# Kernel tuning notes

Hardware: AMD Instinct MI355X
Metric: run time of the kernel (lower is better)

Reference implementation:

```python
import jax, jax.numpy as jnp
import numpy as np

D_MODEL = 1024
N_HEADS = 16
HEAD_DIM = D_MODEL // N_HEADS
B, L = 2, 2048


def setup_inputs() -> dict:
    key = jax.random.key(0)
    ks = jax.random.split(key, 12)
    s = 1.0 / np.sqrt(D_MODEL)
    inp = {
        'q': jax.random.normal(ks[0], (B, L, D_MODEL), dtype=jnp.float32),
        'k': jax.random.normal(ks[1], (B, L, D_MODEL), dtype=jnp.float32),
        'v': jax.random.normal(ks[2], (B, L, D_MODEL), dtype=jnp.float32),
        'Wq': jax.random.uniform(ks[3], (D_MODEL, D_MODEL), jnp.float32, -s, s),
        'bq': jax.random.uniform(ks[4], (D_MODEL,), jnp.float32, -s, s),
        'Wk': jax.random.uniform(ks[5], (D_MODEL, D_MODEL), jnp.float32, -s, s),
        'bk': jax.random.uniform(ks[6], (D_MODEL,), jnp.float32, -s, s),
        'Wv': jax.random.uniform(ks[7], (D_MODEL, D_MODEL), jnp.float32, -s, s),
        'bv': jax.random.uniform(ks[8], (D_MODEL,), jnp.float32, -s, s),
        'Wo': jax.random.uniform(ks[9], (D_MODEL, D_MODEL), jnp.float32, -s, s),
        'bo': jax.random.uniform(ks[10], (D_MODEL,), jnp.float32, -s, s),
    }
    return inp


def _heads(x):
    # (B, L, D) -> (B, H, L, Dh)
    b, l, _ = x.shape
    return x.reshape(b, l, N_HEADS, HEAD_DIM).transpose(0, 2, 1, 3)


def reference(q, k, v, Wq, bq, Wk, bk, Wv, bv, Wo, bo):
    # Linear projections (torch Linear: x @ W.T + b)
    qh = _heads(q @ Wq.T + bq)
    kh = _heads(k @ Wk.T + bk)
    vh = _heads(v @ Wv.T + bv)
    scale = 1.0 / jnp.sqrt(jnp.asarray(HEAD_DIM, dtype=qh.dtype))
    scores = jnp.einsum('bhqd,bhkd->bhqk', qh, kh) * scale  # (B,H,L,L)
    attn = jax.nn.softmax(scores, axis=-1)
    out = jnp.einsum('bhqk,bhkd->bhqd', attn, vh)
    out = out.transpose(0, 2, 1, 3).reshape(q.shape[0], q.shape[1], D_MODEL)
    return out @ Wo.T + bo
```

## Files before the change

### kernel.cpp

```cpp
#include <hip/hip_runtime.h>

typedef unsigned short u16;
typedef __bf16 bf16x8 __attribute__((ext_vector_type(8)));
typedef float f32x4 __attribute__((ext_vector_type(4)));
typedef float f32x16 __attribute__((ext_vector_type(16)));
typedef unsigned short u16x8 __attribute__((ext_vector_type(8)));
typedef unsigned short u16x4 __attribute__((ext_vector_type(4)));

#define LSEQ 2048
#define DM 1024
#define NH 16
#define HD 64
#define SCALE_Q 0.1803368801111244f

__device__ __forceinline__ u16 f2bf(float f) {
  union { float f; unsigned int u; } x;
  x.f = f;
  unsigned int u = x.u;
  u += 0x7FFFu + ((u >> 16) & 1u);
  return (u16)(u >> 16);
}

__device__ __forceinline__ float fexp2(float x) {
  return __builtin_amdgcn_exp2f(x);
}

__device__ __forceinline__ void async16(const void* g, void* l) {
  __builtin_amdgcn_global_load_lds(
      (const __attribute__((address_space(1))) void*)g,
      (__attribute__((address_space(3))) void*)l, 16, 0, 0);
}

__device__ __forceinline__ f32x4 mfma16(bf16x8 a, bf16x8 b, f32x4 c) {
  return __builtin_amdgcn_mfma_f32_16x16x32_bf16(a, b, c, 0, 0, 0);
}
__device__ __forceinline__ f32x16 mfma32(bf16x8 a, bf16x8 b, f32x16 c) {
  return __builtin_amdgcn_mfma_f32_32x32x16_bf16(a, b, c, 0, 0, 0);
}

__device__ __forceinline__ unsigned cvtpk(float lo, float hi) {
  unsigned r;
  asm("v_cvt_pk_bf16_f32 %0, %1, %2" : "=v"(r) : "v"(lo), "v"(hi));
  return r;
}
__device__ __forceinline__ void pswap(unsigned &a, unsigned &b) {
  asm("v_permlane32_swap_b32 %0, %1" : "+v"(a), "+v"(b));
}
__device__ __forceinline__ bf16x8 mk8(unsigned w0, unsigned w1, unsigned w2, unsigned w3) {
  union { unsigned u[4]; bf16x8 v; } x;
  x.u[0] = w0; x.u[1] = w1; x.u[2] = w2; x.u[3] = w3;
  return x.v;
}
__device__ __forceinline__ f32x16 zero16() {
  f32x16 z;
#pragma unroll
  for (int i = 0; i < 16; ++i) z[i] = 0.f;
  return z;
}

__global__ void cvtw(const float* __restrict__ src, u16* __restrict__ dst, int n) {
  const int i = (blockIdx.x * blockDim.x + threadIdx.x) * 4;
  if (i >= n) return;
  f32x4 f = *(const f32x4*)(src + i);
  u16x4 h;
#pragma unroll
  for (int j = 0; j < 4; ++j) h[j] = f2bf(f[j]);
  *(u16x4*)(dst + i) = h;
}

__global__ __launch_bounds__(256) void gemm_qkv(
    const float* __restrict__ xq, const float* __restrict__ xk, const float* __restrict__ xv,
    const u16* __restrict__ Wqb, const u16* __restrict__ Wkb, const u16* __restrict__ Wvb,
    const float* __restrict__ bq, const float* __restrict__ bk, const float* __restrict__ bv,
    u16* __restrict__ Qp, u16* __restrict__ Kp, u16* __restrict__ Vp)
{
  __shared__ __align__(16) u16 As[2][128 * 32];
  __shared__ __align__(16) u16 Bs[2][128 * 32];

  const int tid = threadIdx.x;
  const int lane = tid & 63;
  const int wid = tid >> 6;
  const int lr = lane & 15, lg = lane >> 4;
  const int wr = wid >> 1, wc = wid & 1;
  const int bm = blockIdx.x;
  const int by = blockIdx.y;
  const int wsel = by >> 3;
  const int bn = by & 7;

  const float* A    = (wsel == 0) ? xq  : (wsel == 1) ? xk  : xv;
  const u16*   Bt   = (wsel == 0) ? Wqb : (wsel == 1) ? Wkb : Wvb;
  const float* bias = (wsel == 0) ? bq  : (wsel == 1) ? bk  : bv;
  u16*         Out  = (wsel == 0) ? Qp  : (wsel == 1) ? Kp  : Vp;
  const float oscale = (wsel == 0) ? SCALE_Q : 1.0f;

  const int r0 = tid >> 2;
  const int c0 = (tid & 3) * 8;
  const size_t arow0 = (size_t)(bm * 128 + r0) * DM;
  const size_t arow1 = (size_t)(bm * 128 + 64 + r0) * DM;
  const size_t brow0 = (size_t)(bn * 128 + r0) * DM;
  const size_t brow1 = (size_t)(bn * 128 + 64 + r0) * DM;

  f32x4 acc[4][4];
#pragma unroll
  for (int m = 0; m < 4; ++m)
#pragma unroll
    for (int n = 0; n < 4; ++n) {
      f32x4 z = {0.f, 0.f, 0.f, 0.f};
      acc[m][n] = z;
    }

  {
    async16(Bt + brow0 + c0, &Bs[0][tid * 8]);
    async16(Bt + brow1 + c0, &Bs[0][2048 + tid * 8]);
    const float* g0 = A + arow0 + c0;
    const float* g1 = A + arow1 + c0;
    f32x4 v00 = *(const f32x4*)g0, v01 = *(const f32x4*)(g0 + 4);
    f32x4 v10 = *(const f32x4*)g1, v11 = *(const f32x4*)(g1 + 4);
    u16x8 h0, h1;
#pragma unroll
    for (int j = 0; j < 4; ++j) {
      h0[j] = f2bf(v00[j]); h0[4 + j] = f2bf(v01[j]);
      h1[j] = f2bf(v10[j]); h1[4 + j] = f2bf(v11[j]);
    }
    *(u16x8*)&As[0][tid * 8] = h0;
    *(u16x8*)&As[0][2048 + tid * 8] = h1;
  }
  __syncthreads();

  for (int kt = 0; kt < 32; ++kt) {
    const int cur = kt & 1, nxt = cur ^ 1;
    const bool hn = (kt + 1) < 32;
    f32x4 v00, v01, v10, v11;
    if (hn) {
      const int kk = (kt + 1) * 32;
      async16(Bt + brow0 + kk + c0, &Bs[nxt][tid * 8]);
      async16(Bt + brow1 + kk + c0, &Bs[nxt][2048 + tid * 8]);
      const float* g0 = A + arow0 + kk + c0;
      const float* g1 = A + arow1 + kk + c0;
      v00 = *(const f32x4*)g0; v01 = *(const f32x4*)(g0 + 4);
      v10 = *(const f32x4*)g1; v11 = *(const f32x4*)(g1 + 4);
    }
    bf16x8 af[4], bfr[4];
#pragma unroll
    for (int m = 0; m < 4; ++m)
      af[m] = *(const bf16x8*)&As[cur][(wr * 64 + m * 16 + lr) * 32 + lg * 8];
#pragma unroll
    for (int n = 0; n < 4; ++n)
      bfr[n] = *(const bf16x8*)&Bs[cur][(wc * 64 + n * 16 + lr) * 32 + lg * 8];
#pragma unroll
    for (int m = 0; m < 4; ++m)
#pragma unroll
      for (int n = 0; n < 4; ++n)
        acc[m][n] = mfma16(af[m], bfr[n], acc[m][n]);
    if (hn) {
      u16x8 h0, h1;
#pragma unroll
      for (int j = 0; j < 4; ++j) {
        h0[j] = f2bf(v00[j]); h0[4 + j] = f2bf(v01[j]);
        h1[j] = f2bf(v10[j]); h1[4 + j] = f2bf(v11[j]);
      }
      *(u16x8*)&As[nxt][tid * 8] = h0;
      *(u16x8*)&As[nxt][2048 + tid * 8] = h1;
    }
    __syncthreads();
  }

#pragma unroll
  for (int m = 0; m < 4; ++m) {
#pragma unroll
    for (int n = 0; n < 4; ++n) {
      const int col = bn * 128 + wc * 64 + n * 16 + lr;
      const float bv_ = bias[col];
      const int h = col >> 6, d = col & 63;
#pragma unroll
      for (int r = 0; r < 4; ++r) {
        const int row = bm * 128 + wr * 64 + m * 16 + lg * 4 + r;
        const int b = row >> 11, l = row & 2047;
        Out[((size_t)(b * NH + h) * LSEQ + l) * HD + d] =
            f2bf((acc[m][n][r] + bv_) * oscale);
      }
    }
  }
}

__global__ __launch_bounds__(256) void attn_fwd(
    const u16* __restrict__ Qp, const u16* __restrict__ Kp, const u16* __restrict__ Vp,
    u16* __restrict__ ctx)
{
  __shared__ __align__(16) u16 Ks[2][64 * 64];
  __shared__ __align__(16) u16 Vts[2][64 * 64];

  const int tid = threadIdx.x;
  const int wid = tid >> 6;
  const int lane = tid & 63;
  const int lq = lane & 31;
  const int h = lane >> 5;
  const int qt = blockIdx.x, bh = blockIdx.y;

  const u16* Qb = Qp + (size_t)bh * (LSEQ * HD);
  const u16* Kb = Kp + (size_t)bh * (LSEQ * HD);
  const u16* Vb = Vp + (size_t)bh * (LSEQ * HD);

  const int q0 = qt * 128 + wid * 32;

  bf16x8 qf[4];
#pragma unroll
  for (int dk = 0; dk < 4; ++dk)
    qf[dk] = *(const bf16x8*)(Qb + (size_t)(q0 + lq) * HD + dk * 16 + h * 8);

  float l_run = 0.f;
  f32x16 o0 = zero16(), o1 = zero16();

  const int krow = tid >> 3;
  const int kslot = tid & 7;
  const int ksrc = krow * 64 + ((kslot ^ (krow & 7)) << 3);

  const int kp = tid & 31;
  const int vd0 = (tid >> 5) * 8;

  {
    async16(Kb + ksrc, &Ks[0][tid * 8]);
    async16(Kb + 2048 + ksrc, &Ks[0][2048 + tid * 8]);
    const u16* vsrc = Vb + (size_t)(2 * kp) * HD + vd0;
    u16x8 va = *(const u16x8*)vsrc;
    u16x8 vb_ = *(const u16x8*)(vsrc + HD);
    unsigned int* V32 = (unsigned int*)&Vts[0][0];
#pragma unroll
    for (int i = 0; i < 8; ++i) {
      const int row = vd0 + i;
      V32[row * 32 + (kp ^ ((row & 7) << 2))] =
          (unsigned int)va[i] | ((unsigned int)vb_[i] << 16);
    }
  }
  __syncthreads();

  for (int kt = 0; kt < LSEQ / 64; ++kt) {
    const int cur = kt & 1, nxt = cur ^ 1;
    const bool hn = (kt + 1) < LSEQ / 64;
    u16x8 va, vb_;
    if (hn) {
      async16(Kb + (kt + 1) * 4096 + ksrc, &Ks[nxt][tid * 8]);
      async16(Kb + (kt + 1) * 4096 + 2048 + ksrc, &Ks[nxt][2048 + tid * 8]);
      const u16* vsrc = Vb + (size_t)((kt + 1) * 64 + 2 * kp) * HD + vd0;
      va = *(const u16x8*)vsrc;
      vb_ = *(const u16x8*)(vsrc + HD);
    }

    f32x16 st0 = zero16(), st1 = zero16();
    __builtin_amdgcn_s_setprio(1);
#pragma unroll
    for (int dk = 0; dk < 4; ++dk) {
      const int g = ((2 * dk + h) ^ (lq & 7)) << 3;
      bf16x8 kf0 = *(const bf16x8*)&Ks[cur][lq * 64 + g];
      bf16x8 kf1 = *(const bf16x8*)&Ks[cur][(32 + lq) * 64 + g];
      st0 = mfma32(kf0, qf[dk], st0);
      st1 = mfma32(kf1, qf[dk], st1);
    }
    __builtin_amdgcn_s_setprio(0);

    float rs = 0.f;
#pragma unroll
    for (int i = 0; i < 16; ++i) { st0[i] = fexp2(st0[i]); rs += st0[i]; }
#pragma unroll
    for (int i = 0; i < 16; ++i) { st1[i] = fexp2(st1[i]); rs += st1[i]; }
    l_run += rs;

    unsigned w[16];
#pragma unroll
    for (int m = 0; m < 4; ++m) {
      w[m * 2 + 0] = cvtpk(st0[4 * m + 0], st0[4 * m + 1]);
      w[m * 2 + 1] = cvtpk(st0[4 * m + 2], st0[4 * m + 3]);
      w[8 + m * 2 + 0] = cvtpk(st1[4 * m + 0], st1[4 * m + 1]);
      w[8 + m * 2 + 1] = cvtpk(st1[4 * m + 2], st1[4 * m + 3]);
    }
#pragma unroll
    for (int n = 0; n < 2; ++n) {
      pswap(w[n * 8 + 0], w[n * 8 + 2]);
      pswap(w[n * 8 + 1], w[n * 8 + 3]);
      pswap(w[n * 8 + 4], w[n * 8 + 6]);
      pswap(w[n * 8 + 5], w[n * 8 + 7]);
    }
    bf16x8 pa[4];
    pa[0] = mk8(w[0], w[1], w[2], w[3]);
    pa[1] = mk8(w[4], w[5], w[6], w[7]);
    pa[2] = mk8(w[8], w[9], w[10], w[11]);
    pa[3] = mk8(w[12], w[13], w[14], w[15]);

    __builtin_amdgcn_s_setprio(1);
#pragma unroll
    for (int ks = 0; ks < 4; ++ks) {
      const int g0g = ((2 * ks + h) ^ (lq & 7)) << 3;
      bf16x8 vf0 = *(const bf16x8*)&Vts[cur][lq * 64 + g0g];
      bf16x8 vf1 = *(const bf16x8*)&Vts[cur][(32 + lq) * 64 + g0g];
      o0 = mfma32(pa[ks], vf0, o0);
      o1 = mfma32(pa[ks], vf1, o1);
    }
    __builtin_amdgcn_s_setprio(0);

    if (hn) {
      unsigned int* V32 = (unsigned int*)&Vts[nxt][0];
#pragma unroll
      for (int i = 0; i < 8; ++i) {
        const int row = vd0 + i;
        V32[row * 32 + (kp ^ ((row & 7) << 2))] =
            (unsigned int)va[i] | ((unsigned int)vb_[i] << 16);
      }
    }
    __syncthreads();
  }

  const int b = bh >> 4, head = bh & 15;
  const float ltot = l_run + __shfl_xor(l_run, 32);
  const float linv = 1.0f / ltot;
#pragma unroll
  for (int reg = 0; reg < 16; ++reg) {
    const int row = (reg & 3) + 8 * (reg >> 2) + 4 * h;
    const float iv = __shfl(linv, row);
    const size_t base = ((size_t)(b * LSEQ + q0 + row)) * DM + head * HD;
    ctx[base + lq] = f2bf(o0[reg] * iv);
    ctx[base + 32 + lq] = f2bf(o1[reg] * iv);
  }
}

__global__ __launch_bounds__(256) void gemm_out(
    const u16* __restrict__ Actx, const u16* __restrict__ Wob,
    const float* __restrict__ bo, float* __restrict__ out)
{
  __shared__ __align__(16) u16 As[2][128 * 32];
  __shared__ __align__(16) u16 Bs[2][128 * 32];

  const int tid = threadIdx.x;
  const int lane = tid & 63;
  const int wid = tid >> 6;
  const int lr = lane & 15, lg = lane >> 4;
  const int wr = wid >> 1, wc = wid & 1;
  const int bm = blockIdx.x;
  const int bn = blockIdx.y;

  const int r0 = tid >> 2;
  const int c0 = (tid & 3) * 8;
  const size_t arow0 = (size_t)(bm * 128 + r0) * DM;
  const size_t arow1 = (size_t)(bm * 128 + 64 + r0) * DM;
  const size_t brow0 = (size_t)(bn * 128 + r0) * DM;
  const size_t brow1 = (size_t)(bn * 128 + 64 + r0) * DM;

  f32x4 acc[4][4];
#pragma unroll
  for (int m = 0; m < 4; ++m)
#pragma unroll
    for (int n = 0; n < 4; ++n) {
      f32x4 z = {0.f, 0.f, 0.f, 0.f};
      acc[m][n] = z;
    }

  async16(Actx + arow0 + c0, &As[0][tid * 8]);
  async16(Actx + arow1 + c0, &As[0][2048 + tid * 8]);
  async16(Wob + brow0 + c0, &Bs[0][tid * 8]);
  async16(Wob + brow1 + c0, &Bs[0][2048 + tid * 8]);
  __syncthreads();

  for (int kt = 0; kt < 32; ++kt) {
    const int cur = kt & 1, nxt = cur ^ 1;
    if (kt + 1 < 32) {
      const int kk = (kt + 1) * 32;
      async16(Actx + arow0 + kk + c0, &As[nxt][tid * 8]);
      async16(Actx + arow1 + kk + c0, &As[nxt][2048 + tid * 8]);
      async16(Wob + brow0 + kk + c0, &Bs[nxt][tid * 8]);
      async16(Wob + brow1 + kk + c0, &Bs[nxt][2048 + tid * 8]);
    }
    bf16x8 af[4], bfr[4];
#pragma unroll
    for (int m = 0; m < 4; ++m)
      af[m] = *(const bf16x8*)&As[cur][(wr * 64 + m * 16 + lr) * 32 + lg * 8];
#pragma unroll
    for (int n = 0; n < 4; ++n)
      bfr[n] = *(const bf16x8*)&Bs[cur][(wc * 64 + n * 16 + lr) * 32 + lg * 8];
#pragma unroll
    for (int m = 0; m < 4; ++m)
#pragma unroll
      for (int n = 0; n < 4; ++n)
        acc[m][n] = mfma16(af[m], bfr[n], acc[m][n]);
    __syncthreads();
  }

#pragma unroll
  for (int m = 0; m < 4; ++m) {
#pragma unroll
    for (int n = 0; n < 4; ++n) {
      const int col = bn * 128 + wc * 64 + n * 16 + lr;
      const float bv_ = bo[col];
#pragma unroll
      for (int r = 0; r < 4; ++r) {
        const int row = bm * 128 + wr * 64 + m * 16 + lg * 4 + r;
        out[(size_t)row * DM + col] = acc[m][n][r] + bv_;
      }
    }
  }
}

extern "C" void kernel_launch(void* const* d_in, const int* in_sizes, int n_in,
                              void* d_out, int out_size, void* d_ws, size_t ws_size,
                              hipStream_t stream) {
  const float* q  = (const float*)d_in[0];
  const float* k  = (const float*)d_in[1];
  const float* v  = (const float*)d_in[2];
  const float* Wq = (const float*)d_in[3];
  const float* bq = (const float*)d_in[4];
  const float* Wk = (const float*)d_in[5];
  const float* bk = (const float*)d_in[6];
  const float* Wv = (const float*)d_in[7];
  const float* bv = (const float*)d_in[8];
  const float* Wo = (const float*)d_in[9];
  const float* bo = (const float*)d_in[10];
  float* out = (float*)d_out;

  u16* ws  = (u16*)d_ws;
  u16* Wqb = ws;
  u16* Wkb = Wqb + (1u << 20);
  u16* Wvb = Wkb + (1u << 20);
  u16* Wob = Wvb + (1u << 20);
  u16* Qp  = Wob + (1u << 20);
  u16* Kp  = Qp + (4u << 20);
  u16* Vp  = Kp + (4u << 20);
  u16* ctx = Vp + (4u << 20);

  cvtw<<<1024, 256, 0, stream>>>(Wq, Wqb, 1 << 20);
  cvtw<<<1024, 256, 0, stream>>>(Wk, Wkb, 1 << 20);
  cvtw<<<1024, 256, 0, stream>>>(Wv, Wvb, 1 << 20);
  cvtw<<<1024, 256, 0, stream>>>(Wo, Wob, 1 << 20);
  gemm_qkv<<<dim3(32, 24), 256, 0, stream>>>(q, k, v, Wqb, Wkb, Wvb,
                                             bq, bk, bv, Qp, Kp, Vp);
  attn_fwd<<<dim3(16, 32), 256, 0, stream>>>(Qp, Kp, Vp, ctx);
  gemm_out<<<dim3(32, 8), 256, 0, stream>>>(ctx, Wob, bo, out);
}
```

Before: 145.5 us.

## Write V transposed from projection GEMM and load it with async copies

The QKV projection now writes V directly in a transposed per-head layout (d-major, sequence contiguous) with packed bf16 stores. The attention kernel then fetches V tiles with the same swizzled async global-to-LDS copies used for K, instead of loading rows into registers and scattering transposed 32-bit writes into LDS every iteration. Separately, fp32-to-bf16 conversion in cvtw and in the GEMM A staging uses the packed hardware convert instruction and handles 8 elements per thread. The cost is strided 8-byte global stores for V in the GEMM epilogue. The packed convert may also round differently from the software round-to-nearest-even helper.

```diff
diff --git a/kernel.cpp b/kernel.cpp
--- a/kernel.cpp
+++ b/kernel.cpp
@@ -6,6 +6,8 @@
 typedef float f32x16 __attribute__((ext_vector_type(16)));
 typedef unsigned short u16x8 __attribute__((ext_vector_type(8)));
 typedef unsigned short u16x4 __attribute__((ext_vector_type(4)));
+typedef unsigned int u32x2 __attribute__((ext_vector_type(2)));
+typedef unsigned int u32x4 __attribute__((ext_vector_type(4)));
 
 #define LSEQ 2048
 #define DM 1024
@@ -57,22 +59,26 @@
   for (int i = 0; i < 16; ++i) z[i] = 0.f;
   return z;
 }
+__device__ __forceinline__ void pack8(const f32x4& a, const f32x4& b, void* dst) {
+  u32x4 w;
+  w[0] = cvtpk(a[0], a[1]); w[1] = cvtpk(a[2], a[3]);
+  w[2] = cvtpk(b[0], b[1]); w[3] = cvtpk(b[2], b[3]);
+  *(u32x4*)dst = w;
+}
 
 __global__ void cvtw(const float* __restrict__ src, u16* __restrict__ dst, int n) {
-  const int i = (blockIdx.x * blockDim.x + threadIdx.x) * 4;
+  const int i = (blockIdx.x * blockDim.x + threadIdx.x) * 8;
   if (i >= n) return;
-  f32x4 f = *(const f32x4*)(src + i);
-  u16x4 h;
-#pragma unroll
-  for (int j = 0; j < 4; ++j) h[j] = f2bf(f[j]);
-  *(u16x4*)(dst + i) = h;
+  f32x4 f0 = *(const f32x4*)(src + i);
+  f32x4 f1 = *(const f32x4*)(src + i + 4);
+  pack8(f0, f1, dst + i);
 }
 
 __global__ __launch_bounds__(256) void gemm_qkv(
     const float* __restrict__ xq, const float* __restrict__ xk, const float* __restrict__ xv,
     const u16* __restrict__ Wqb, const u16* __restrict__ Wkb, const u16* __restrict__ Wvb,
     const float* __restrict__ bq, const float* __restrict__ bk, const float* __restrict__ bv,
-    u16* __restrict__ Qp, u16* __restrict__ Kp, u16* __restrict__ Vp)
+    u16* __restrict__ Qp, u16* __restrict__ Kp, u16* __restrict__ Vt)
 {
   __shared__ __align__(16) u16 As[2][128 * 32];
   __shared__ __align__(16) u16 Bs[2][128 * 32];
@@ -90,8 +96,6 @@
   const float* A    = (wsel == 0) ? xq  : (wsel == 1) ? xk  : xv;
   const u16*   Bt   = (wsel == 0) ? Wqb : (wsel == 1) ? Wkb : Wvb;
   const float* bias = (wsel == 0) ? bq  : (wsel == 1) ? bk  : bv;
-  u16*         Out  = (wsel == 0) ? Qp  : (wsel == 1) ? Kp  : Vp;
-  const float oscale = (wsel == 0) ? SCALE_Q : 1.0f;
 
   const int r0 = tid >> 2;
   const int c0 = (tid & 3) * 8;
@@ -116,14 +120,8 @@
     const float* g1 = A + arow1 + c0;
     f32x4 v00 = *(const f32x4*)g0, v01 = *(const f32x4*)(g0 + 4);
     f32x4 v10 = *(const f32x4*)g1, v11 = *(const f32x4*)(g1 + 4);
-    u16x8 h0, h1;
-#pragma unroll
-    for (int j = 0; j < 4; ++j) {
-      h0[j] = f2bf(v00[j]); h0[4 + j] = f2bf(v01[j]);
-      h1[j] = f2bf(v10[j]); h1[4 + j] = f2bf(v11[j]);
-    }
-    *(u16x8*)&As[0][tid * 8] = h0;
-    *(u16x8*)&As[0][2048 + tid * 8] = h1;
+    pack8(v00, v01, &As[0][tid * 8]);
+    pack8(v10, v11, &As[0][2048 + tid * 8]);
   }
   __syncthreads();
 
@@ -153,38 +151,53 @@
       for (int n = 0; n < 4; ++n)
         acc[m][n] = mfma16(af[m], bfr[n], acc[m][n]);
     if (hn) {
-      u16x8 h0, h1;
-#pragma unroll
-      for (int j = 0; j < 4; ++j) {
-        h0[j] = f2bf(v00[j]); h0[4 + j] = f2bf(v01[j]);
-        h1[j] = f2bf(v10[j]); h1[4 + j] = f2bf(v11[j]);
+      pack8(v00, v01, &As[nxt][tid * 8]);
+      pack8(v10, v11, &As[nxt][2048 + tid * 8]);
+    }
+    __syncthreads();
+  }
+
+  if (wsel < 2) {
+    u16* Out = (wsel == 0) ? Qp : Kp;
+    const float oscale = (wsel == 0) ? SCALE_Q : 1.0f;
+#pragma unroll
+    for (int m = 0; m < 4; ++m) {
+#pragma unroll
+      for (int n = 0; n < 4; ++n) {
+        const int col = bn * 128 + wc * 64 + n * 16 + lr;
+        const float bv_ = bias[col];
+        const int h = col >> 6, d = col & 63;
+#pragma unroll
+        for (int r = 0; r < 4; ++r) {
+          const int row = bm * 128 + wr * 64 + m * 16 + lg * 4 + r;
+          const int b = row >> 11, l = row & 2047;
+          Out[((size_t)(b * NH + h) * LSEQ + l) * HD + d] =
+              f2bf((acc[m][n][r] + bv_) * oscale);
+        }
       }
-      *(u16x8*)&As[nxt][tid * 8] = h0;
-      *(u16x8*)&As[nxt][2048 + tid * 8] = h1;
-    }
-    __syncthreads();
-  }
-
-#pragma unroll
-  for (int m = 0; m < 4; ++m) {
-#pragma unroll
-    for (int n = 0; n < 4; ++n) {
-      const int col = bn * 128 + wc * 64 + n * 16 + lr;
-      const float bv_ = bias[col];
-      const int h = col >> 6, d = col & 63;
-#pragma unroll
-      for (int r = 0; r < 4; ++r) {
-        const int row = bm * 128 + wr * 64 + m * 16 + lg * 4 + r;
-        const int b = row >> 11, l = row & 2047;
-        Out[((size_t)(b * NH + h) * LSEQ + l) * HD + d] =
-            f2bf((acc[m][n][r] + bv_) * oscale);
+    }
+  } else {
+    const int row0b = bm * 128 + wr * 64 + lg * 4;
+    const int b = (bm * 128) >> 11;
+#pragma unroll
+    for (int m = 0; m < 4; ++m) {
+      const int l0 = (row0b + m * 16) & 2047;
+#pragma unroll
+      for (int n = 0; n < 4; ++n) {
+        const int col = bn * 128 + wc * 64 + n * 16 + lr;
+        const float bv_ = bias[col];
+        const int h = col >> 6, d = col & 63;
+        u32x2 w;
+        w[0] = cvtpk(acc[m][n][0] + bv_, acc[m][n][1] + bv_);
+        w[1] = cvtpk(acc[m][n][2] + bv_, acc[m][n][3] + bv_);
+        *(u32x2*)&Vt[((size_t)(b * NH + h) * HD + d) * LSEQ + l0] = w;
       }
     }
   }
 }
 
 __global__ __launch_bounds__(256) void attn_fwd(
-    const u16* __restrict__ Qp, const u16* __restrict__ Kp, const u16* __restrict__ Vp,
+    const u16* __restrict__ Qp, const u16* __restrict__ Kp, const u16* __restrict__ Vt,
     u16* __restrict__ ctx)
 {
   __shared__ __align__(16) u16 Ks[2][64 * 64];
@@ -199,7 +212,7 @@
 
   const u16* Qb = Qp + (size_t)bh * (LSEQ * HD);
   const u16* Kb = Kp + (size_t)bh * (LSEQ * HD);
-  const u16* Vb = Vp + (size_t)bh * (LSEQ * HD);
+  const u16* Vb = Vt + (size_t)bh * (HD * LSEQ);
 
   const int q0 = qt * 128 + wid * 32;
 
@@ -211,39 +224,29 @@
   float l_run = 0.f;
   f32x16 o0 = zero16(), o1 = zero16();
 
-  const int krow = tid >> 3;
-  const int kslot = tid & 7;
-  const int ksrc = krow * 64 + ((kslot ^ (krow & 7)) << 3);
-
-  const int kp = tid & 31;
-  const int vd0 = (tid >> 5) * 8;
+  const int srow = tid >> 3;
+  const int sslot = tid & 7;
+  const int sswz = (sslot ^ (srow & 7)) << 3;
+  const int ksrc = srow * 64 + sswz;
+  const size_t vsrc0 = (size_t)srow * LSEQ + sswz;
+  const size_t vsrc1 = (size_t)(srow + 32) * LSEQ + sswz;
 
   {
     async16(Kb + ksrc, &Ks[0][tid * 8]);
     async16(Kb + 2048 + ksrc, &Ks[0][2048 + tid * 8]);
-    const u16* vsrc = Vb + (size_t)(2 * kp) * HD + vd0;
-    u16x8 va = *(const u16x8*)vsrc;
-    u16x8 vb_ = *(const u16x8*)(vsrc + HD);
-    unsigned int* V32 = (unsigned int*)&Vts[0][0];
-#pragma unroll
-    for (int i = 0; i < 8; ++i) {
-      const int row = vd0 + i;
-      V32[row * 32 + (kp ^ ((row & 7) << 2))] =
-          (unsigned int)va[i] | ((unsigned int)vb_[i] << 16);
-    }
+    async16(Vb + vsrc0, &Vts[0][tid * 8]);
+    async16(Vb + vsrc1, &Vts[0][2048 + tid * 8]);
   }
   __syncthreads();
 
   for (int kt = 0; kt < LSEQ / 64; ++kt) {
     const int cur = kt & 1, nxt = cur ^ 1;
     const bool hn = (kt + 1) < LSEQ / 64;
-    u16x8 va, vb_;
     if (hn) {
       async16(Kb + (kt + 1) * 4096 + ksrc, &Ks[nxt][tid * 8]);
       async16(Kb + (kt + 1) * 4096 + 2048 + ksrc, &Ks[nxt][2048 + tid * 8]);
-      const u16* vsrc = Vb + (size_t)((kt + 1) * 64 + 2 * kp) * HD + vd0;
-      va = *(const u16x8*)vsrc;
-      vb_ = *(const u16x8*)(vsrc + HD);
+      async16(Vb + (kt + 1) * 64 + vsrc0, &Vts[nxt][tid * 8]);
+      async16(Vb + (kt + 1) * 64 + vsrc1, &Vts[nxt][2048 + tid * 8]);
     }
 
     f32x16 st0 = zero16(), st1 = zero16();
@@ -297,15 +300,6 @@
     }
     __builtin_amdgcn_s_setprio(0);
 
-    if (hn) {
-      unsigned int* V32 = (unsigned int*)&Vts[nxt][0];
-#pragma unroll
-      for (int i = 0; i < 8; ++i) {
-        const int row = vd0 + i;
-        V32[row * 32 + (kp ^ ((row & 7) << 2))] =
-            (unsigned int)va[i] | ((unsigned int)vb_[i] << 16);
-      }
-    }
     __syncthreads();
   }
 
@@ -421,15 +415,15 @@
   u16* Wob = Wvb + (1u << 20);
   u16* Qp  = Wob + (1u << 20);
   u16* Kp  = Qp + (4u << 20);
-  u16* Vp  = Kp + (4u << 20);
-  u16* ctx = Vp + (4u << 20);
-
-  cvtw<<<1024, 256, 0, stream>>>(Wq, Wqb, 1 << 20);
-  cvtw<<<1024, 256, 0, stream>>>(Wk, Wkb, 1 << 20);
-  cvtw<<<1024, 256, 0, stream>>>(Wv, Wvb, 1 << 20);
-  cvtw<<<1024, 256, 0, stream>>>(Wo, Wob, 1 << 20);
+  u16* Vt  = Kp + (4u << 20);
+  u16* ctx = Vt + (4u << 20);
+
+  cvtw<<<512, 256, 0, stream>>>(Wq, Wqb, 1 << 20);
+  cvtw<<<512, 256, 0, stream>>>(Wk, Wkb, 1 << 20);
+  cvtw<<<512, 256, 0, stream>>>(Wv, Wvb, 1 << 20);
+  cvtw<<<512, 256, 0, stream>>>(Wo, Wob, 1 << 20);
   gemm_qkv<<<dim3(32, 24), 256, 0, stream>>>(q, k, v, Wqb, Wkb, Wvb,
-                                             bq, bk, bv, Qp, Kp, Vp);
-  attn_fwd<<<dim3(16, 32), 256, 0, stream>>>(Qp, Kp, Vp, ctx);
+                                             bq, bk, bv, Qp, Kp, Vt);
+  attn_fwd<<<dim3(16, 32), 256, 0, stream>>>(Qp, Kp, Vt, ctx);
   gemm_out<<<dim3(32, 8), 256, 0, stream>>>(ctx, Wob, bo, out);
 }
```

After: 159.8 us. 9.8% more time.
